# Kernel optimization log

Measured on AMD Instinct MI355X. Metric: run time of the kernel, lower is better.

Reference implementation:

```python
import jax, jax.numpy as jnp
import numpy as np
from jax.scipy.special import logsumexp

B, T, D = 256, 2048, 64


def setup_inputs() -> dict:
    key = jax.random.key(0)
    k1, k2, k3, k4 = jax.random.split(key, 4)
    p = jax.random.normal(k1, (B, T, D), dtype=jnp.float32)
    labels = jax.random.randint(k2, (B, T), 0, D)
    y = jax.nn.one_hot(labels, D, dtype=jnp.int32)  # [B,T,D] one-hot labels
    # valid lengths in [T//2, T]; mask == 1 marks padding positions
    lengths = jax.random.randint(k3, (B,), T // 2, T + 1)
    mask = (jnp.arange(T)[None, :] >= lengths[:, None]).astype(jnp.int32)
    transition = 0.1 * jax.random.normal(k4, (D, D), dtype=jnp.float32)
    return {"p": p, "y": y, "mask": mask, "transition": transition}


def reference(p, y, mask, transition):
    # CRF negative log-likelihood per example: logZ - emission_score - transition_score
    Bb = p.shape[0]
    valid = (1 - mask).astype(jnp.float32)            # [B,T], 1 = valid token
    y1 = y.astype(jnp.float32) * valid[:, :, None]    # masked one-hot labels
    s1 = jnp.sum(y1 * p, axis=(1, 2))                 # emission score
    pair = jnp.einsum('btd,bte->bde', y1[:, :-1], y1[:, 1:])  # label bigram counts
    s2 = jnp.sum(pair * transition, axis=(1, 2))      # transition score

    # forward algorithm: alpha_t = p_t + logsumexp(alpha_{t-1}[:, :, None] + T)
    def step(state, inp):
        new = inp + logsumexp(state[:, :, None] + transition[None, :, :], axis=1)
        return new, new

    xs = jnp.moveaxis(p[:, 1:, :], 1, 0)              # [T-1, B, D]
    _, a1 = jax.lax.scan(step, p[:, 0, :], xs)        # a1: [T-1, B, D]

    # index of alpha at the last valid timestep (length L -> a1 index L-2)
    m1 = jnp.argmin(
        jnp.concatenate([valid.astype(jnp.int32), jnp.zeros((Bb, 1), jnp.int32)], axis=1),
        axis=1) - 2                                   # [B]
    last = a1[m1, jnp.arange(Bb)]                     # [B, D]
    logZ = logsumexp(last, axis=-1)
    return logZ - s1 - s2
```

## Files before the change

### kernel.cpp

```cpp
#include <hip/hip_runtime.h>
#include <stdint.h>
#include <string.h>

#define BB 256
#define TT 2048
#define DD 64
#define CC 64
#define SS 32
#define C_L2E 1.44269504f
#define C_LN2 0.69314718f
#define C_BIAS 0.0028174f

typedef short sh8  __attribute__((ext_vector_type(8)));
typedef float f32x4 __attribute__((ext_vector_type(4)));

union BU { sh8 v8; unsigned int u[4]; unsigned short s[8]; };

__device__ __forceinline__ float expf_fast(float x) { return __builtin_amdgcn_exp2f(x * C_L2E); }
__device__ __forceinline__ unsigned short bf16rne(float x) {
    unsigned int u = __float_as_uint(x);
    u += 0x7FFF + ((u >> 16) & 1u);
    return (unsigned short)(u >> 16);
}
__device__ __forceinline__ unsigned int pkbf(float hi, float lo) {
    return __builtin_amdgcn_perm(__float_as_uint(hi), __float_as_uint(lo), 0x07060302u);
}

#define DPPMAX(x, ctrl, rm, bm) { int _xi = __float_as_int(x);                              \
    int _yi = __builtin_amdgcn_update_dpp(_xi, _xi, ctrl, rm, bm, false);                   \
    x = fmaxf(x, __int_as_float(_yi)); }

__global__ __launch_bounds__(256) void crf_len(
    const int* __restrict__ mask, int* __restrict__ wsL)
{
    __shared__ int r4[4];
    const int c = blockIdx.x, tid = threadIdx.x;
    const int4* mrow = (const int4*)(mask + (size_t)c * TT);
    int4 a = mrow[tid * 2], b = mrow[tid * 2 + 1];
    int s = a.x + a.y + a.z + a.w + b.x + b.y + b.z + b.w;
#pragma unroll
    for (int xm = 32; xm >= 1; xm >>= 1) s += __shfl_xor(s, xm, 64);
    if ((tid & 63) == 0) r4[tid >> 6] = s;
    __syncthreads();
    if (tid == 0) wsL[c] = TT - (r4[0] + r4[1] + r4[2] + r4[3]);
}

__global__ __launch_bounds__(256) void crf_lab(
    const int* __restrict__ y, unsigned char* __restrict__ labsG)
{
    const int tid = threadIdx.x;
    const int g = tid & 15, sub = tid >> 4;
    const size_t base = (size_t)blockIdx.x * 64;
    int4 v[4];
#pragma unroll
    for (int k = 0; k < 4; ++k)
        v[k] = ((const int4*)y)[(base + (size_t)k * 16 + sub) * 16 + g];
#pragma unroll
    for (int k = 0; k < 4; ++k) {
        int s = v[k].x * (4 * g) + v[k].y * (4 * g + 1)
              + v[k].z * (4 * g + 2) + v[k].w * (4 * g + 3);
#pragma unroll
        for (int xm = 1; xm <= 8; xm <<= 1) s += __shfl_xor(s, xm, 16);
        if (g == 0) labsG[base + k * 16 + sub] = (unsigned char)s;
    }
}

__global__ __launch_bounds__(256) void crf_gth(
    const float* __restrict__ p, const unsigned char* __restrict__ labsG,
    const int* __restrict__ mask, const float* __restrict__ tr,
    float* __restrict__ wsS)
{
    __shared__ float redf[4];
    const int c = blockIdx.y, t0 = blockIdx.x * 256;
    const int tid = threadIdx.x;
    const size_t cb = (size_t)c * TT;
    const int tt = t0 + tid;

    const int m0 = mask[cb + tt];
    const int m1 = (tt + 1 < TT) ? mask[cb + tt + 1] : 1;
    const int l0 = labsG[cb + tt];

    float s = 0.f;
    if (m0 == 0)
        s += p[(cb + tt) * DD + l0];
    if (m1 == 0) {
        const int l1 = labsG[cb + tt + 1];
        s += tr[l0 * DD + l1];
    }
#pragma unroll
    for (int xm = 32; xm >= 1; xm >>= 1) s += __shfl_xor(s, xm, 64);
    if ((tid & 63) == 0) redf[tid >> 6] = s;
    __syncthreads();
    if (tid == 0)
        atomicAdd(&wsS[c], redf[0] + redf[1] + redf[2] + redf[3]);
}

__global__ __launch_bounds__(256) void crf_probe(
    const float* __restrict__ p, const float* __restrict__ tr,
    const int* __restrict__ wsL,
    unsigned short* __restrict__ wsA, unsigned short* __restrict__ wsB, int* __restrict__ wsSig)
{
    const int tid = threadIdx.x, w = tid >> 6, lane = tid & 63;
    const int q = lane >> 4, ml = lane & 15;
    const int cg = blockIdx.x;
    const int ic = blockIdx.y * 2 + (w >> 1);
    const int bwd = w & 1;
    const int c = cg * 16 + ml;
    const int Lml = wsL[c];
    const int t0 = ic * SS, t1 = t0 + SS;
    const int ts = (ic == 0) ? 1 : t0;
    const float* prow = p + (size_t)c * TT * DD;

    BU A[4][2];
#pragma unroll
    for (int mt = 0; mt < 4; ++mt)
#pragma unroll
        for (int kt2 = 0; kt2 < 2; ++kt2)
#pragma unroll
            for (int j = 0; j < 8; ++j) {
                int lam = 32 * kt2 + 16 * (j >> 2) + 4 * q + (j & 3);
                float tv = bwd ? tr[(16 * mt + ml) * DD + lam] : tr[lam * DD + 16 * mt + ml];
                A[mt][kt2].s[j] = (short)bf16rne(expf_fast(tv));
            }

    float xs[16];
    if (!bwd && ic == 0) {
#pragma unroll
        for (int k = 0; k < 4; ++k) {
            f32x4 v = *(const f32x4*)(prow + 16 * k + 4 * q);
#pragma unroll
            for (int r = 0; r < 4; ++r)
                xs[(k >> 1) * 8 + (k & 1) * 4 + r] = __builtin_amdgcn_exp2f(fmaf(v[r], C_L2E, C_BIAS));
        }
    } else {
#pragma unroll
        for (int i = 0; i < 16; ++i) xs[i] = 1.0f;
    }

    int mL = Lml;
#pragma unroll
    for (int xm = 32; xm >= 1; xm >>= 1) { int o = __shfl_xor(mL, xm, 64); mL = o > mL ? o : mL; }
    int ibeg = 0, iend = SS;
    if (!bwd) { int ir = mL - t0; if (ir < 0) ir = 0; iend = (ir + 3) & ~3; if (iend > SS) iend = SS; }
    else      { int ir = t1 - mL; if (ir < 0) ir = 0; ibeg = ir & ~3; if (ibeg > SS) ibeg = SS; }

    int sig = 0;
    const f32x4 z4 = {0.f, 0.f, 0.f, 0.f};

    if (ibeg < iend) {
        f32x4 er[2][4];
#pragma unroll
        for (int s = 0; s < 2; ++s) {
            int i = ibeg + s;
            int t = bwd ? (t1 - 1 - i) : (t0 + i);
#pragma unroll
            for (int k = 0; k < 4; ++k)
                er[s][k] = *(const f32x4*)(prow + (size_t)t * DD + 16 * k + 4 * q);
        }
        for (int ib = ibeg; ib < iend; ib += 4) {
#pragma unroll
            for (int s = 0; s < 4; ++s) {
                const int i = ib + s;
                const int t = bwd ? (t1 - 1 - i) : (t0 + i);
                const bool act = (t >= ts) && (t < Lml);
                float ee[4][4];
#pragma unroll
                for (int k = 0; k < 4; ++k)
#pragma unroll
                    for (int r = 0; r < 4; ++r)
                        ee[k][r] = __builtin_amdgcn_exp2f(fmaf(er[s & 1][k][r], C_L2E, C_BIAS));
                {
                    int ipf = i + 2;
                    int tpf = bwd ? (t1 - 1 - ipf) : (t0 + ipf);
                    if (tpf < t0) tpf = t0;
                    if (tpf > t1 - 1) tpf = t1 - 1;
#pragma unroll
                    for (int k = 0; k < 4; ++k)
                        er[s & 1][k] = *(const f32x4*)(prow + (size_t)tpf * DD + 16 * k + 4 * q);
                }
                float cand[16];
                BU Bf[2];
                f32x4 acc[4];
                if (!bwd) {
#pragma unroll
                    for (int kt2 = 0; kt2 < 2; ++kt2)
#pragma unroll
                        for (int jj = 0; jj < 4; ++jj)
                            Bf[kt2].u[jj] = pkbf(xs[kt2 * 8 + 2 * jj + 1], xs[kt2 * 8 + 2 * jj]);
#pragma unroll
                    for (int mt = 0; mt < 4; ++mt) {
                        acc[mt] = __builtin_amdgcn_mfma_f32_16x16x32_bf16(A[mt][0].v8, Bf[0].v8, z4, 0, 0, 0);
                        acc[mt] = __builtin_amdgcn_mfma_f32_16x16x32_bf16(A[mt][1].v8, Bf[1].v8, acc[mt], 0, 0, 0);
                    }
#pragma unroll
                    for (int mt = 0; mt < 4; ++mt)
#pragma unroll
                        for (int r = 0; r < 4; ++r)
                            cand[(mt >> 1) * 8 + (mt & 1) * 4 + r] = acc[mt][r] * ee[mt][r];
                } else {
                    float xsc[16];
#pragma unroll
                    for (int kt2 = 0; kt2 < 2; ++kt2)
#pragma unroll
                        for (int h = 0; h < 2; ++h)
#pragma unroll
                            for (int r = 0; r < 4; ++r)
                                xsc[kt2 * 8 + h * 4 + r] = xs[kt2 * 8 + h * 4 + r] * ee[2 * kt2 + h][r];
#pragma unroll
                    for (int kt2 = 0; kt2 < 2; ++kt2)
#pragma unroll
                        for (int jj = 0; jj < 4; ++jj)
                            Bf[kt2].u[jj] = pkbf(xsc[kt2 * 8 + 2 * jj + 1], xsc[kt2 * 8 + 2 * jj]);
#pragma unroll
                    for (int mt = 0; mt < 4; ++mt) {
                        acc[mt] = __builtin_amdgcn_mfma_f32_16x16x32_bf16(A[mt][0].v8, Bf[0].v8, z4, 0, 0, 0);
                        acc[mt] = __builtin_amdgcn_mfma_f32_16x16x32_bf16(A[mt][1].v8, Bf[1].v8, acc[mt], 0, 0, 0);
                    }
#pragma unroll
                    for (int mt = 0; mt < 4; ++mt)
#pragma unroll
                        for (int r = 0; r < 4; ++r)
                            cand[(mt >> 1) * 8 + (mt & 1) * 4 + r] = acc[mt][r];
                }
                if (s == 3) {
                    float mx = fabsf(cand[0]);
#pragma unroll
                    for (int i2 = 1; i2 < 16; ++i2) mx = fmaxf(mx, fabsf(cand[i2]));
                    DPPMAX(mx, 0x111, 0xF, 0xF); DPPMAX(mx, 0x112, 0xF, 0xF);
                    DPPMAX(mx, 0x114, 0xF, 0xF); DPPMAX(mx, 0x118, 0xF, 0xF);
                    DPPMAX(mx, 0x142, 0xA, 0xF); DPPMAX(mx, 0x143, 0xC, 0xF);
                    int smx = __builtin_amdgcn_readlane(__float_as_int(mx), 63);
                    int kk = ((smx >> 23) & 255) - 127;
                    kk = kk < -124 ? -124 : (kk > 124 ? 124 : kk);
                    float sc = __int_as_float((unsigned)(127 - kk) << 23);
#pragma unroll
                    for (int i2 = 0; i2 < 16; ++i2) cand[i2] *= sc;
                    if (act) sig += kk;
                }
#pragma unroll
                for (int i2 = 0; i2 < 16; ++i2) xs[i2] = act ? cand[i2] : xs[i2];
            }
        }
    }

    unsigned short* dst = (bwd ? wsB : wsA) + ((size_t)c * CC + ic) * 64;
#pragma unroll
    for (int kt2 = 0; kt2 < 2; ++kt2)
#pragma unroll
        for (int h = 0; h < 2; ++h)
#pragma unroll
            for (int r = 0; r < 4; ++r)
                dst[32 * kt2 + 16 * h + 4 * q + r] = bf16rne(xs[kt2 * 8 + h * 4 + r]);
    if (!bwd && q == 0) wsSig[c * CC + ic] = sig;
}

__global__ __launch_bounds__(256) void crf_combine(
    const unsigned short* __restrict__ wsA, const unsigned short* __restrict__ wsB,
    const int* __restrict__ wsSig, const float* __restrict__ wsS,
    float* __restrict__ out)
{
    __shared__ float eParts[4];
    const int tid = threadIdx.x, w = tid >> 6, lane = tid & 63;
    const int c = blockIdx.x;

    float Ep = 0.f;
#pragma unroll
    for (int k = 0; k < 16; ++k) {
        const int i = w * 16 + k;
        if (i == 0) continue;
        float b  = __uint_as_float((unsigned)wsB[((size_t)c * CC + i) * 64 + lane] << 16);
        float ap = __uint_as_float((unsigned)wsA[((size_t)c * CC + i - 1) * 64 + lane] << 16);
        float d1 = b * ap, d0 = b;
#pragma unroll
        for (int xm = 32; xm >= 1; xm >>= 1) { d1 += __shfl_xor(d1, xm, 64); d0 += __shfl_xor(d0, xm, 64); }
        Ep += (float)wsSig[c * CC + i] + __builtin_amdgcn_logf(d1) - __builtin_amdgcn_logf(d0);
    }
    if (w == 0) Ep += (float)wsSig[c * CC];
    if (w == 3) {
        float al = __uint_as_float((unsigned)wsA[((size_t)c * CC + CC - 1) * 64 + lane] << 16);
#pragma unroll
        for (int xm = 32; xm >= 1; xm >>= 1) al += __shfl_xor(al, xm, 64);
        Ep += __builtin_amdgcn_logf(al);
    }
    if (lane == 0) eParts[w] = Ep;
    __syncthreads();
    if (tid == 0) {
        float E = eParts[0] + eParts[1] + eParts[2] + eParts[3];
        out[c] = C_LN2 * E - wsS[c];
    }
}

extern "C" void kernel_launch(void* const* d_in, const int* in_sizes, int n_in,
                              void* d_out, int out_size, void* d_ws, size_t ws_size,
                              hipStream_t stream) {
    const float* p  = (const float*)d_in[0];
    const int*   y  = (const int*)d_in[1];
    const int*   mk = (const int*)d_in[2];
    const float* tr = (const float*)d_in[3];
    float* out = (float*)d_out;

    float* wsS  = (float*)d_ws;
    int*   wsL  = (int*)((char*)d_ws + 1024);
    int*   wsSg = (int*)((char*)d_ws + 4096);
    unsigned char* wsLb = (unsigned char*)((char*)d_ws + 131072);
    unsigned short* wsA = (unsigned short*)((char*)d_ws + (1u << 20));
    unsigned short* wsB = (unsigned short*)((char*)d_ws + (3u << 20));

    hipMemsetAsync(d_ws, 0, 1024, stream);
    crf_len<<<dim3(BB), dim3(256), 0, stream>>>(mk, wsL);
    crf_lab<<<dim3(BB * TT / 64), dim3(256), 0, stream>>>(y, wsLb);
    crf_probe<<<dim3(16, CC / 2), dim3(256), 0, stream>>>(p, tr, wsL, wsA, wsB, wsSg);
    crf_gth<<<dim3(8, BB), dim3(256), 0, stream>>>(p, wsLb, mk, tr, wsS);
    crf_combine<<<dim3(BB), dim3(256), 0, stream>>>(wsA, wsB, wsSg, wsS, out);
}
```

Measured before the change: 312.2 us.

## Stage emission rows through swizzled LDS for coalesced global loads

In the probe kernel, each lane previously read its emission fragment straight from global memory in the MFMA layout, which spreads a wavefront's accesses across 16 sequence rows. Now each wave loads whole contiguous 256-byte rows per sequence with coalesced global reads. It writes them into an XOR-swizzled, double-buffered per-wave LDS tile and reads them back in the MFMA fragment layout. This trades scattered global access for extra LDS traffic and 32KB of shared memory per block, which may lower occupancy and adds latency to the serial recurrence.

```diff
diff --git a/kernel.cpp b/kernel.cpp
--- a/kernel.cpp
+++ b/kernel.cpp
@@ -100,6 +100,7 @@
     const int* __restrict__ wsL,
     unsigned short* __restrict__ wsA, unsigned short* __restrict__ wsB, int* __restrict__ wsSig)
 {
+    __shared__ char lds[4][2][4096];
     const int tid = threadIdx.x, w = tid >> 6, lane = tid & 63;
     const int q = lane >> 4, ml = lane & 15;
     const int cg = blockIdx.x;
@@ -111,6 +112,19 @@
     const int ts = (ic == 0) ? 1 : t0;
     const float* prow = p + (size_t)c * TT * DD;
 
+    const int m4 = lane >> 4, u = lane & 15;
+    const float* pb[4];
+    int wr[4], rd[4];
+#pragma unroll
+    for (int k = 0; k < 4; ++k) {
+        const int m = 4 * k + m4;
+        const int su = (u ^ (m & 7)) << 4;
+        pb[k] = p + (size_t)(cg * 16 + m) * TT * DD + (su >> 2);
+        wr[k] = m * 256 + su;
+        rd[k] = ml * 256 + (((4 * k + q) ^ (ml & 7)) << 4);
+    }
+    char* lbase = &lds[w][0][0];
+
     BU A[4][2];
 #pragma unroll
     for (int mt = 0; mt < 4; ++mt)
@@ -148,99 +162,128 @@
     const f32x4 z4 = {0.f, 0.f, 0.f, 0.f};
 
     if (ibeg < iend) {
-        f32x4 er[2][4];
-#pragma unroll
-        for (int s = 0; s < 2; ++s) {
-            int i = ibeg + s;
-            int t = bwd ? (t1 - 1 - i) : (t0 + i);
+        f32x4 gA[4], gB[4];
+        {
+            const int tp0 = bwd ? (t1 - 1 - ibeg) : (t0 + ibeg);
+            f32x4 g0[4];
 #pragma unroll
             for (int k = 0; k < 4; ++k)
-                er[s][k] = *(const f32x4*)(prow + (size_t)t * DD + 16 * k + 4 * q);
+                g0[k] = *(const f32x4*)(pb[k] + (size_t)tp0 * DD);
+            int i1 = ibeg + 1;
+            int tp1 = bwd ? (t1 - 1 - i1) : (t0 + i1);
+            if (tp1 < t0) tp1 = t0;
+            if (tp1 > t1 - 1) tp1 = t1 - 1;
+#pragma unroll
+            for (int k = 0; k < 4; ++k)
+                gB[k] = *(const f32x4*)(pb[k] + (size_t)tp1 * DD);
+#pragma unroll
+            for (int k = 0; k < 4; ++k)
+                *(f32x4*)(lbase + wr[k]) = g0[k];
         }
+
+#define PSTEP(SE, RLOAD, RWRITE)                                                            \
+        {                                                                                   \
+            const int i = ib + SE;                                                          \
+            const int t = bwd ? (t1 - 1 - i) : (t0 + i);                                    \
+            const bool act = (t >= ts) && (t < Lml);                                        \
+            {                                               \
+                int ipf = i + 2;                                                            \
+                int tpf = bwd ? (t1 - 1 - ipf) : (t0 + ipf);                                \
+                if (tpf < t0) tpf = t0;                                                     \
+                if (tpf > t1 - 1) tpf = t1 - 1;                                             \
+                _Pragma("unroll")                                                           \
+                for (int k = 0; k < 4; ++k)                                                 \
+                    RLOAD[k] = *(const f32x4*)(pb[k] + (size_t)tpf * DD);                    \
+            }                                                                               \
+            f32x4 er[4];                                                                    \
+            {                                  \
+                char* lb = lbase + ((SE & 1) * 4096);                                       \
+                _Pragma("unroll")                                                           \
+                for (int k = 0; k < 4; ++k)                                                 \
+                    er[k] = *(const f32x4*)(lb + rd[k]);                                    \
+            }                                                                               \
+            float ee[4][4];                                                                 \
+            _Pragma("unroll")                                                               \
+            for (int k = 0; k < 4; ++k)                                                     \
+                _Pragma("unroll")                                                           \
+                for (int r = 0; r < 4; ++r)                                                 \
+                    ee[k][r] = __builtin_amdgcn_exp2f(fmaf(er[k][r], C_L2E, C_BIAS));       \
+            float cand[16];                                                                 \
+            BU Bf[2];                                                                       \
+            f32x4 acc[4];                                                                   \
+            if (!bwd) {                           \
+                _Pragma("unroll")                                                           \
+                for (int kt2 = 0; kt2 < 2; ++kt2)                                           \
+                    _Pragma("unroll")                                                       \
+                    for (int jj = 0; jj < 4; ++jj)                                          \
+                        Bf[kt2].u[jj] = pkbf(xs[kt2 * 8 + 2 * jj + 1], xs[kt2 * 8 + 2 * jj]); \
+                _Pragma("unroll")                                                           \
+                for (int mt = 0; mt < 4; ++mt) {                                            \
+                    acc[mt] = __builtin_amdgcn_mfma_f32_16x16x32_bf16(A[mt][0].v8, Bf[0].v8, z4, 0, 0, 0); \
+                    acc[mt] = __builtin_amdgcn_mfma_f32_16x16x32_bf16(A[mt][1].v8, Bf[1].v8, acc[mt], 0, 0, 0); \
+                }                                                                           \
+                _Pragma("unroll")                                                           \
+                for (int mt = 0; mt < 4; ++mt)                                              \
+                    _Pragma("unroll")                                                       \
+                    for (int r = 0; r < 4; ++r)                                             \
+                        cand[(mt >> 1) * 8 + (mt & 1) * 4 + r] = acc[mt][r] * ee[mt][r];    \
+            } else {                                  \
+                float xsc[16];                                                              \
+                _Pragma("unroll")                                                           \
+                for (int kt2 = 0; kt2 < 2; ++kt2)                                           \
+                    _Pragma("unroll")                                                       \
+                    for (int h = 0; h < 2; ++h)                                             \
+                        _Pragma("unroll")                                                   \
+                        for (int r = 0; r < 4; ++r)                                         \
+                            xsc[kt2 * 8 + h * 4 + r] = xs[kt2 * 8 + h * 4 + r] * ee[2 * kt2 + h][r]; \
+                _Pragma("unroll")                                                           \
+                for (int kt2 = 0; kt2 < 2; ++kt2)                                           \
+                    _Pragma("unroll")                                                       \
+                    for (int jj = 0; jj < 4; ++jj)                                          \
+                        Bf[kt2].u[jj] = pkbf(xsc[kt2 * 8 + 2 * jj + 1], xsc[kt2 * 8 + 2 * jj]); \
+                _Pragma("unroll")                                                           \
+                for (int mt = 0; mt < 4; ++mt) {                                            \
+                    acc[mt] = __builtin_amdgcn_mfma_f32_16x16x32_bf16(A[mt][0].v8, Bf[0].v8, z4, 0, 0, 0); \
+                    acc[mt] = __builtin_amdgcn_mfma_f32_16x16x32_bf16(A[mt][1].v8, Bf[1].v8, acc[mt], 0, 0, 0); \
+                }                                                                           \
+                _Pragma("unroll")                                                           \
+                for (int mt = 0; mt < 4; ++mt)                                              \
+                    _Pragma("unroll")                                                       \
+                    for (int r = 0; r < 4; ++r)                                             \
+                        cand[(mt >> 1) * 8 + (mt & 1) * 4 + r] = acc[mt][r];                \
+            }                                                                               \
+            {                    \
+                char* lw = lbase + ((1 - (SE & 1)) * 4096);                                 \
+                _Pragma("unroll")                                                           \
+                for (int k = 0; k < 4; ++k)                                                 \
+                    *(f32x4*)(lw + wr[k]) = RWRITE[k];                                      \
+            }                                                                               \
+            if (SE == 3) {                    \
+                float mx = fabsf(cand[0]);                                                  \
+                _Pragma("unroll")                                                           \
+                for (int i2 = 1; i2 < 16; ++i2) mx = fmaxf(mx, fabsf(cand[i2]));            \
+                DPPMAX(mx, 0x111, 0xF, 0xF); DPPMAX(mx, 0x112, 0xF, 0xF);                   \
+                DPPMAX(mx, 0x114, 0xF, 0xF); DPPMAX(mx, 0x118, 0xF, 0xF);                   \
+                DPPMAX(mx, 0x142, 0xA, 0xF); DPPMAX(mx, 0x143, 0xC, 0xF);                   \
+                int smx = __builtin_amdgcn_readlane(__float_as_int(mx), 63);                \
+                int kk = ((smx >> 23) & 255) - 127;                                         \
+                kk = kk < -124 ? -124 : (kk > 124 ? 124 : kk);                              \
+                float sc = __int_as_float((unsigned)(127 - kk) << 23);                      \
+                _Pragma("unroll")                                                           \
+                for (int i2 = 0; i2 < 16; ++i2) cand[i2] *= sc;                             \
+                if (act) sig += kk;                                                         \
+            }                                                                               \
+            _Pragma("unroll")                                                               \
+            for (int i2 = 0; i2 < 16; ++i2) xs[i2] = act ? cand[i2] : xs[i2];               \
+        }
+
         for (int ib = ibeg; ib < iend; ib += 4) {
-#pragma unroll
-            for (int s = 0; s < 4; ++s) {
-                const int i = ib + s;
-                const int t = bwd ? (t1 - 1 - i) : (t0 + i);
-                const bool act = (t >= ts) && (t < Lml);
-                float ee[4][4];
-#pragma unroll
-                for (int k = 0; k < 4; ++k)
-#pragma unroll
-                    for (int r = 0; r < 4; ++r)
-                        ee[k][r] = __builtin_amdgcn_exp2f(fmaf(er[s & 1][k][r], C_L2E, C_BIAS));
-                {
-                    int ipf = i + 2;
-                    int tpf = bwd ? (t1 - 1 - ipf) : (t0 + ipf);
-                    if (tpf < t0) tpf = t0;
-                    if (tpf > t1 - 1) tpf = t1 - 1;
-#pragma unroll
-                    for (int k = 0; k < 4; ++k)
-                        er[s & 1][k] = *(const f32x4*)(prow + (size_t)tpf * DD + 16 * k + 4 * q);
-                }
-                float cand[16];
-                BU Bf[2];
-                f32x4 acc[4];
-                if (!bwd) {
-#pragma unroll
-                    for (int kt2 = 0; kt2 < 2; ++kt2)
-#pragma unroll
-                        for (int jj = 0; jj < 4; ++jj)
-                            Bf[kt2].u[jj] = pkbf(xs[kt2 * 8 + 2 * jj + 1], xs[kt2 * 8 + 2 * jj]);
-#pragma unroll
-                    for (int mt = 0; mt < 4; ++mt) {
-                        acc[mt] = __builtin_amdgcn_mfma_f32_16x16x32_bf16(A[mt][0].v8, Bf[0].v8, z4, 0, 0, 0);
-                        acc[mt] = __builtin_amdgcn_mfma_f32_16x16x32_bf16(A[mt][1].v8, Bf[1].v8, acc[mt], 0, 0, 0);
-                    }
-#pragma unroll
-                    for (int mt = 0; mt < 4; ++mt)
-#pragma unroll
-                        for (int r = 0; r < 4; ++r)
-                            cand[(mt >> 1) * 8 + (mt & 1) * 4 + r] = acc[mt][r] * ee[mt][r];
-                } else {
-                    float xsc[16];
-#pragma unroll
-                    for (int kt2 = 0; kt2 < 2; ++kt2)
-#pragma unroll
-                        for (int h = 0; h < 2; ++h)
-#pragma unroll
-                            for (int r = 0; r < 4; ++r)
-                                xsc[kt2 * 8 + h * 4 + r] = xs[kt2 * 8 + h * 4 + r] * ee[2 * kt2 + h][r];
-#pragma unroll
-                    for (int kt2 = 0; kt2 < 2; ++kt2)
-#pragma unroll
-                        for (int jj = 0; jj < 4; ++jj)
-                            Bf[kt2].u[jj] = pkbf(xsc[kt2 * 8 + 2 * jj + 1], xsc[kt2 * 8 + 2 * jj]);
-#pragma unroll
-                    for (int mt = 0; mt < 4; ++mt) {
-                        acc[mt] = __builtin_amdgcn_mfma_f32_16x16x32_bf16(A[mt][0].v8, Bf[0].v8, z4, 0, 0, 0);
-                        acc[mt] = __builtin_amdgcn_mfma_f32_16x16x32_bf16(A[mt][1].v8, Bf[1].v8, acc[mt], 0, 0, 0);
-                    }
-#pragma unroll
-                    for (int mt = 0; mt < 4; ++mt)
-#pragma unroll
-                        for (int r = 0; r < 4; ++r)
-                            cand[(mt >> 1) * 8 + (mt & 1) * 4 + r] = acc[mt][r];
-                }
-                if (s == 3) {
-                    float mx = fabsf(cand[0]);
-#pragma unroll
-                    for (int i2 = 1; i2 < 16; ++i2) mx = fmaxf(mx, fabsf(cand[i2]));
-                    DPPMAX(mx, 0x111, 0xF, 0xF); DPPMAX(mx, 0x112, 0xF, 0xF);
-                    DPPMAX(mx, 0x114, 0xF, 0xF); DPPMAX(mx, 0x118, 0xF, 0xF);
-                    DPPMAX(mx, 0x142, 0xA, 0xF); DPPMAX(mx, 0x143, 0xC, 0xF);
-                    int smx = __builtin_amdgcn_readlane(__float_as_int(mx), 63);
-                    int kk = ((smx >> 23) & 255) - 127;
-                    kk = kk < -124 ? -124 : (kk > 124 ? 124 : kk);
-                    float sc = __int_as_float((unsigned)(127 - kk) << 23);
-#pragma unroll
-                    for (int i2 = 0; i2 < 16; ++i2) cand[i2] *= sc;
-                    if (act) sig += kk;
-                }
-#pragma unroll
-                for (int i2 = 0; i2 < 16; ++i2) xs[i2] = act ? cand[i2] : xs[i2];
-            }
+            PSTEP(0, gA, gB)
+            PSTEP(1, gB, gA)
+            PSTEP(2, gA, gB)
+            PSTEP(3, gB, gA)
         }
+#undef PSTEP
     }
 
     unsigned short* dst = (bwd ? wsB : wsA) + ((size_t)c * CC + ic) * 64;
```

Result: no change. 317.7 us (+1.8%).
